# Kernel optimization log

Hardware: AMD Instinct MI355X
Metric: run time of the kernel (lower is better)

The kernel has to match this reference:

```python
import jax, jax.numpy as jnp
import numpy as np

NUM_HEADS = 16

def setup_inputs() -> dict:
    key = jax.random.key(0)
    k1, k2, k3 = jax.random.split(key, 3)
    B, S, D = 4, 2048, 1024
    x = jax.random.normal(k1, (B, S, D), dtype=jnp.float32)
    # xavier-uniform-like small init so unscaled logits stay numerically sane
    w_qkv = jax.random.normal(k2, (3 * D, D), dtype=jnp.float32) * 0.02
    w_out = jax.random.normal(k3, (D, D), dtype=jnp.float32) * 0.02
    return {"x": x, "w_qkv": w_qkv, "w_out": w_out}

def reference(x, w_qkv, w_out):
    B, S, D = x.shape
    H = NUM_HEADS
    d = D // H
    # qkv projection (Linear, no bias): x @ W^T -> [B, S, 3D]
    qkv = jnp.einsum('bsd,ed->bse', x, w_qkv).reshape(B, S, H, 3 * d)
    q, k, v = jnp.split(qkv, 3, axis=-1)           # each [B, S, H, d]
    q = q.transpose(0, 2, 1, 3)                    # [B, H, S, d]
    k = k.transpose(0, 2, 1, 3)
    v = v.transpose(0, 2, 1, 3)
    # NOTE: the original module does NOT scale by 1/sqrt(d) — faithful.
    logits = jnp.einsum('bhqd,bhkd->bhqk', q, k)   # [B, H, S, S]
    attn = jax.nn.softmax(logits, axis=-1)
    vals = jnp.einsum('bhqk,bhkd->bhqd', attn, v)  # [B, H, S, d]
    vals = vals.transpose(0, 2, 1, 3).reshape(B, S, D)
    return jnp.einsum('bsd,od->bso', vals, w_out)
```

## Files before the change

kernel.cpp:

```cpp
#include <hip/hip_runtime.h>
#include <hip/hip_bf16.h>

#define DEVINL __device__ __forceinline__

typedef short bf16x4 __attribute__((ext_vector_type(4)));
typedef short bf16x8 __attribute__((ext_vector_type(8)));
typedef float f32x4 __attribute__((ext_vector_type(4)));
typedef float f32x16 __attribute__((ext_vector_type(16)));
typedef unsigned short us4 __attribute__((ext_vector_type(4)));


DEVINL unsigned short f2bf(float f) {
  unsigned u = __builtin_bit_cast(unsigned, f);
  unsigned r = u + 0x7fffu + ((u >> 16) & 1u);
  return (unsigned short)(r >> 16);
}

DEVINL f32x4 mfma32(bf16x8 a, bf16x8 b, f32x4 c) {
  return __builtin_amdgcn_mfma_f32_16x16x32_bf16(a, b, c, 0, 0, 0);
}

DEVINL f32x16 mfma3216(bf16x8 a, bf16x8 b, f32x16 c) {
  return __builtin_amdgcn_mfma_f32_32x32x16_bf16(a, b, c, 0, 0, 0);
}

DEVINL float fexp2(float x) {
#if __has_builtin(__builtin_amdgcn_exp2f)
  return __builtin_amdgcn_exp2f(x);
#else
  return exp2f(x);
#endif
}

DEVINL unsigned cvt_pk_bf16(float a, float b) {
  unsigned r;
  asm("v_cvt_pk_bf16_f32 %0, %1, %2" : "=v"(r) : "v"(a), "v"(b));
  return r;
}

DEVINL void permswap(unsigned& x, unsigned& y) {
#if __has_builtin(__builtin_amdgcn_permlane32_swap)
  typedef int i32x2_t __attribute__((ext_vector_type(2)));
  i32x2_t r = __builtin_amdgcn_permlane32_swap((int)x, (int)y, false, false);
  x = (unsigned)r[0];
  y = (unsigned)r[1];
#else
  asm("v_permlane32_swap_b32 %0, %1" : "+v"(x), "+v"(y));
#endif
}

#define GLOAD_LDS16(g, l)                                                    \
  __builtin_amdgcn_global_load_lds(                                          \
      (__attribute__((address_space(1))) void*)(unsigned short*)(g),         \
      (__attribute__((address_space(3))) void*)(l), 16, 0, 0)

__global__ void cvtk(const float* __restrict__ src,
                     unsigned short* __restrict__ dst, int n4) {
  int i = blockIdx.x * 256 + threadIdx.x;
  const int st = gridDim.x * 256;
  for (; i < n4; i += st) {
    const float4 v = ((const float4*)src)[i];
    us4 o;
    o[0] = f2bf(v.x); o[1] = f2bf(v.y); o[2] = f2bf(v.z); o[3] = f2bf(v.w);
    ((us4*)dst)[i] = o;
  }
}

__global__ __launch_bounds__(256, 2) void qkv_gemm(
    const unsigned short* __restrict__ A,
    const unsigned short* __restrict__ Bw,
    unsigned short* __restrict__ Qo,
    unsigned short* __restrict__ Ko,
    unsigned short* __restrict__ VTo) {
  constexpr int K = 1024;
  __shared__ unsigned short SH[16384];
  const int tid = threadIdx.x;
  const int lane = tid & 63;
  const int wid = tid >> 6;
  const int l15 = lane & 15, g = lane >> 4;
  const int fid = blockIdx.y * 24 + blockIdx.x;
  const int swzid = (fid & 7) * 192 + (fid >> 3);
  const int m0 = (swzid / 24) * 128;
  const int n0 = (swzid % 24) * 128;
  const int wr = wid >> 1, wc = wid & 1;

  f32x4 acc[4][4] = {};

  const int sidx0 = tid * 8;
  const int sidx1 = (256 + tid) * 8;
  const int r0 = sidx0 >> 5, c0 = sidx0 & 31;
  const int r1 = sidx1 >> 5, c1 = sidx1 & 31;

#define QSTAGE(kt, bb)                                                       \
  {                                                                          \
    const int k0_ = (kt)*32;                                                 \
    GLOAD_LDS16(A + (size_t)(m0 + r0) * K + k0_ + c0,                        \
                SH + (bb)*8192 + sidx0);                                     \
    GLOAD_LDS16(Bw + (size_t)(n0 + r0) * K + k0_ + c0,                       \
                SH + (bb)*8192 + 4096 + sidx0);                              \
    GLOAD_LDS16(A + (size_t)(m0 + r1) * K + k0_ + c1,                        \
                SH + (bb)*8192 + sidx1);                                     \
    GLOAD_LDS16(Bw + (size_t)(n0 + r1) * K + k0_ + c1,                       \
                SH + (bb)*8192 + 4096 + sidx1);                              \
  }

  QSTAGE(0, 0);
  __syncthreads();

  for (int t = 0; t < 32; ++t) {
    const int cb = t & 1;
    if (t < 31) QSTAGE(t + 1, cb ^ 1);
    bf16x8 af[4], bfr[4];
#pragma unroll
    for (int i = 0; i < 4; ++i) {
      af[i] =
          *(const bf16x8*)(SH + cb * 8192 + (wr * 64 + i * 16 + l15) * 32 +
                           g * 8);
      bfr[i] = *(const bf16x8*)(SH + cb * 8192 + 4096 +
                                (wc * 64 + i * 16 + l15) * 32 + g * 8);
    }
#pragma unroll
    for (int mi = 0; mi < 4; ++mi)
#pragma unroll
      for (int ni = 0; ni < 4; ++ni)
        acc[mi][ni] = mfma32(af[mi], bfr[ni], acc[mi][ni]);
    __syncthreads();
  }
#undef QSTAGE

#pragma unroll
  for (int ni = 0; ni < 4; ++ni) {
    const int ebase = n0 + wc * 64 + ni * 16;
    const int h = ebase / 192;
    const int rbase = ebase - h * 192;
#pragma unroll
    for (int mi = 0; mi < 4; ++mi) {
      const int mbase = m0 + wr * 64 + mi * 16 + g * 4;
      if (rbase >= 128) {
        const int rv = rbase + l15 - 128;
        const int b = mbase >> 11, s = mbase & 2047;
        const int bh = b * 16 + h;
        us4 ov;
#pragma unroll
        for (int j = 0; j < 4; ++j) ov[j] = f2bf(acc[mi][ni][j]);
        *(us4*)(VTo + ((size_t)bh * 64 + rv) * 2048 + s) = ov;
      } else {
        const float scale = (rbase < 64) ? 1.44269504f : 1.0f;
        const int eloc = wc * 64 + ni * 16 + l15;
        const int mloc = wr * 64 + mi * 16 + g * 4;
#pragma unroll
        for (int j = 0; j < 4; ++j)
          SH[(mloc + j) * 128 + eloc] = f2bf(acc[mi][ni][j] * scale);
      }
    }
  }
  __syncthreads();
#pragma unroll
  for (int k = 0; k < 8; ++k) {
    const int c = tid + k * 256;
    const int ml = c >> 4, e8 = (c & 15) * 8;
    const int e0 = n0 + e8;
    const int h = e0 / 192;
    const int r = e0 - h * 192;
    if (r < 128) {
      const int mm = m0 + ml;
      const int b = mm >> 11, s = mm & 2047;
      const int bh = b * 16 + h;
      const bf16x8 v = *(const bf16x8*)&SH[ml * 128 + e8];
      if (r < 64)
        *(bf16x8*)(Qo + ((size_t)bh * 2048 + s) * 64 + r) = v;
      else
        *(bf16x8*)(Ko + ((size_t)bh * 2048 + s) * 64 + (r - 64)) = v;
    }
  }
}

__global__ __launch_bounds__(256, 2) void attn_fwd(
    const unsigned short* __restrict__ Q,
    const unsigned short* __restrict__ K,
    const unsigned short* __restrict__ VT,
    unsigned short* __restrict__ Vals) {
  __shared__ unsigned short Ks[2][128 * 64];
  __shared__ unsigned short Vs[2][64 * 128];
  __shared__ float invs[4][2][32];
  const int tid = threadIdx.x;
  const int lane = tid & 63;
  const int wid = tid >> 6;
  const int l31 = lane & 31;
  const int hi = lane >> 5;
  const int bid = (blockIdx.x & 7) * 64 + (blockIdx.x >> 3);
  const int bh = bid >> 3;
  const int q0 = (bid & 7) * 256 + wid * 64;
  const unsigned short* Qb = Q + (size_t)bh * (2048 * 64);
  const unsigned short* Kb = K + (size_t)bh * (2048 * 64);
  const unsigned short* Vb = VT + (size_t)bh * (64 * 2048);

  bf16x8 qf[2][4];
#pragma unroll
  for (int qt = 0; qt < 2; ++qt) {
    const unsigned short* qrow = Qb + (size_t)(q0 + qt * 32 + l31) * 64;
#pragma unroll
    for (int kw = 0; kw < 4; ++kw)
      qf[qt][kw] = *(const bf16x8*)(qrow + kw * 16 + hi * 8);
  }

  float lsum[2] = {0.0f, 0.0f};
  f32x16 o[2][2] = {};
  const unsigned swz = (unsigned)((l31 & 7) << 4);
  const unsigned laneK = (unsigned)(l31 * 128) + (((unsigned)hi << 4) ^ swz);
  const unsigned laneV = (unsigned)(l31 * 256) + (((unsigned)hi << 4) ^ swz);

#define STAGE(kv0, nb)                                                       \
  {                                                                          \
    _Pragma("unroll") for (int j = 0; j < 4; ++j) {                          \
      const int c = tid + j * 256;                                           \
      const int kr = c >> 3;                                                 \
      const int ksc = ((((c & 7) << 4) ^ ((kr & 7) << 4)) >> 1);             \
      GLOAD_LDS16(Kb + (size_t)((kv0) + kr) * 64 + ksc, &Ks[nb][c * 8]);     \
      const int vr = c >> 4;                                                 \
      const int vsc = ((((c & 15) << 4) ^ ((vr & 7) << 4)) >> 1);            \
      GLOAD_LDS16(Vb + (size_t)vr * 2048 + (kv0) + vsc, &Vs[nb][c * 8]);     \
    }                                                                        \
  }

  STAGE(0, 0);
  __syncthreads();

  for (int kv0 = 0; kv0 < 2048; kv0 += 128) {
    const int cur = (kv0 >> 7) & 1;
    if (kv0 + 128 < 2048) STAGE(kv0 + 128, cur ^ 1);
    const char* kb = (const char*)Ks[cur];
    const char* vb = (const char*)Vs[cur];
#pragma unroll
    for (int sub = 0; sub < 4; ++sub) {
      const unsigned kbase = laneK + (unsigned)(sub * 4096);
      bf16x8 kf[4];
#pragma unroll
      for (int kw = 0; kw < 4; ++kw)
        kf[kw] = *(const bf16x8*)(kb + (kbase ^ (unsigned)(kw * 32)));
      f32x16 s0 = {}, s1 = {};
      __builtin_amdgcn_s_setprio(1);
#pragma unroll
      for (int kw = 0; kw < 4; ++kw) s0 = mfma3216(kf[kw], qf[0][kw], s0);
#pragma unroll
      for (int kw = 0; kw < 4; ++kw) s1 = mfma3216(kf[kw], qf[1][kw], s1);
      __builtin_amdgcn_s_setprio(0);
#pragma unroll
      for (int half = 0; half < 2; ++half) {
        const int pb = half * 8;
        const unsigned ksoff = (unsigned)((sub * 2 + half) * 32);
        const bf16x8 vf0 = *(const bf16x8*)(vb + (laneV ^ ksoff));
        const bf16x8 vf1 = *(const bf16x8*)(vb + ((laneV + 8192u) ^ ksoff));
#pragma unroll
        for (int qt = 0; qt < 2; ++qt) {
          const f32x16& s = qt ? s1 : s0;
          const float p0 = fexp2(s[pb + 0]);
          const float p1 = fexp2(s[pb + 1]);
          const float p2 = fexp2(s[pb + 2]);
          const float p3 = fexp2(s[pb + 3]);
          const float p4 = fexp2(s[pb + 4]);
          const float p5 = fexp2(s[pb + 5]);
          const float p6 = fexp2(s[pb + 6]);
          const float p7 = fexp2(s[pb + 7]);
          lsum[qt] += ((p0 + p1) + (p2 + p3)) + ((p4 + p5) + (p6 + p7));
          unsigned w0 = cvt_pk_bf16(p0, p1);
          unsigned w2 = cvt_pk_bf16(p4, p5);
          permswap(w0, w2);
          unsigned w1 = cvt_pk_bf16(p2, p3);
          unsigned w3 = cvt_pk_bf16(p6, p7);
          permswap(w1, w3);
          union {
            unsigned u[4];
            bf16x8 v;
          } pk;
          pk.u[0] = w0;
          pk.u[1] = w1;
          pk.u[2] = w2;
          pk.u[3] = w3;
          __builtin_amdgcn_s_setprio(1);
          o[qt][0] = mfma3216(pk.v, vf0, o[qt][0]);
          o[qt][1] = mfma3216(pk.v, vf1, o[qt][1]);
          __builtin_amdgcn_s_setprio(0);
        }
      }
    }
    __syncthreads();
  }
#undef STAGE

#pragma unroll
  for (int qt = 0; qt < 2; ++qt) {
    const float ltot = lsum[qt] + __shfl_xor(lsum[qt], 32);
    invs[wid][qt][l31] = 1.0f / ltot;
  }
  const int b = bh >> 4, h = bh & 15;
#pragma unroll
  for (int qt = 0; qt < 2; ++qt) {
    unsigned short* ob =
        Vals + (size_t)(b * 2048 + q0 + qt * 32) * 1024 + h * 64 + l31;
#pragma unroll
    for (int j = 0; j < 16; ++j) {
      const int ql = (j & 3) + 8 * (j >> 2) + 4 * hi;
      const float inv = invs[wid][qt][ql];
      ob[(size_t)ql * 1024] = f2bf(o[qt][0][j] * inv);
      ob[(size_t)ql * 1024 + 32] = f2bf(o[qt][1][j] * inv);
    }
  }
}

__global__ __launch_bounds__(256, 2) void out_gemm(
    const unsigned short* __restrict__ A,
    const unsigned short* __restrict__ Bw,
    float* __restrict__ C) {
  constexpr int K = 1024, BK = 32;
  __shared__ unsigned short As[128 * BK];
  __shared__ unsigned short Bs[128 * BK];
  const int tid = threadIdx.x;
  const int lane = tid & 63;
  const int wid = tid >> 6;
  const int l15 = lane & 15, g = lane >> 4;
  const int fid = blockIdx.y * 8 + blockIdx.x;
  const int swzid = (fid & 7) * 64 + (fid >> 3);
  const int m0 = (swzid >> 3) * 128;
  const int n0 = (swzid & 7) * 128;
  const int wr = wid >> 1, wc = wid & 1;

  f32x4 acc[4][4] = {};

  const int sidx0 = tid * 8;
  const int sidx1 = (256 + tid) * 8;
  const int r0 = sidx0 >> 5, c0 = sidx0 & 31;
  const int r1 = sidx1 >> 5, c1 = sidx1 & 31;

  for (int k0 = 0; k0 < K; k0 += BK) {
    __syncthreads();
    GLOAD_LDS16(A + (size_t)(m0 + r0) * K + k0 + c0, As + sidx0);
    GLOAD_LDS16(Bw + (size_t)(n0 + r0) * K + k0 + c0, Bs + sidx0);
    GLOAD_LDS16(A + (size_t)(m0 + r1) * K + k0 + c1, As + sidx1);
    GLOAD_LDS16(Bw + (size_t)(n0 + r1) * K + k0 + c1, Bs + sidx1);
    __syncthreads();
    bf16x8 af[4], bfr[4];
#pragma unroll
    for (int i = 0; i < 4; ++i) {
      af[i] = *(const bf16x8*)(As + (wr * 64 + i * 16 + l15) * BK + g * 8);
      bfr[i] = *(const bf16x8*)(Bs + (wc * 64 + i * 16 + l15) * BK + g * 8);
    }
#pragma unroll
    for (int mi = 0; mi < 4; ++mi)
#pragma unroll
      for (int ni = 0; ni < 4; ++ni)
        acc[mi][ni] = mfma32(af[mi], bfr[ni], acc[mi][ni]);
  }

#pragma unroll
  for (int mi = 0; mi < 4; ++mi) {
    const int mbase = m0 + wr * 64 + mi * 16 + g * 4;
#pragma unroll
    for (int ni = 0; ni < 4; ++ni) {
      const int n = n0 + wc * 64 + ni * 16 + l15;
#pragma unroll
      for (int j = 0; j < 4; ++j)
        C[(size_t)(mbase + j) * 1024 + n] = acc[mi][ni][j];
    }
  }
}

extern "C" void kernel_launch(void* const* d_in, const int* in_sizes, int n_in,
                              void* d_out, int out_size, void* d_ws,
                              size_t ws_size, hipStream_t stream) {
  const float* x = (const float*)d_in[0];
  const float* w_qkv = (const float*)d_in[1];
  const float* w_out = (const float*)d_in[2];
  float* out = (float*)d_out;

  char* ws = (char*)d_ws;
  unsigned short* xb = (unsigned short*)(ws);
  unsigned short* wqkvb = (unsigned short*)(ws + (16u << 20));
  unsigned short* woutb = (unsigned short*)(ws + (22u << 20));
  unsigned short* Qt = (unsigned short*)(ws + (24u << 20));
  unsigned short* Kt = (unsigned short*)(ws + (40u << 20));
  unsigned short* VTt = (unsigned short*)(ws + (56u << 20));
  unsigned short* vals = xb;

  cvtk<<<2048, 256, 0, stream>>>(x, xb, 8388608 / 4);
  cvtk<<<2048, 256, 0, stream>>>(w_qkv, wqkvb, 3145728 / 4);
  cvtk<<<1024, 256, 0, stream>>>(w_out, woutb, 1048576 / 4);
  qkv_gemm<<<dim3(24, 64), 256, 0, stream>>>(xb, wqkvb, Qt, Kt, VTt);
  attn_fwd<<<512, 256, 0, stream>>>(Qt, Kt, VTt, vals);
  out_gemm<<<dim3(8, 64), 256, 0, stream>>>(vals, woutb, out);
}
```

Baseline: 186.5 us.

## Use eight waves per attention block with one 32-row query tile each

The attention kernel moves from 4 waves each handling two 32-row query tiles to 8 waves each handling one 32-row tile. The block still covers 256 query rows and shares the same K/V LDS staging, now split across 512 threads. Per-wave register use drops, so more waves can be resident to hide latency. The cost is more waves contending for LDS reads and barriers, and the K fragments loaded from LDS are reused over half as many query rows.

```diff
diff --git a/kernel.cpp b/kernel.cpp
--- a/kernel.cpp
+++ b/kernel.cpp
@@ -175,14 +175,14 @@
   }
 }
 
-__global__ __launch_bounds__(256, 2) void attn_fwd(
+__global__ __launch_bounds__(512, 4) void attn_fwd(
     const unsigned short* __restrict__ Q,
     const unsigned short* __restrict__ K,
     const unsigned short* __restrict__ VT,
     unsigned short* __restrict__ Vals) {
   __shared__ unsigned short Ks[2][128 * 64];
   __shared__ unsigned short Vs[2][64 * 128];
-  __shared__ float invs[4][2][32];
+  __shared__ float invs[8][32];
   const int tid = threadIdx.x;
   const int lane = tid & 63;
   const int wid = tid >> 6;
@@ -190,30 +190,27 @@
   const int hi = lane >> 5;
   const int bid = (blockIdx.x & 7) * 64 + (blockIdx.x >> 3);
   const int bh = bid >> 3;
-  const int q0 = (bid & 7) * 256 + wid * 64;
+  const int q0 = (bid & 7) * 256 + wid * 32;
   const unsigned short* Qb = Q + (size_t)bh * (2048 * 64);
   const unsigned short* Kb = K + (size_t)bh * (2048 * 64);
   const unsigned short* Vb = VT + (size_t)bh * (64 * 2048);
 
-  bf16x8 qf[2][4];
-#pragma unroll
-  for (int qt = 0; qt < 2; ++qt) {
-    const unsigned short* qrow = Qb + (size_t)(q0 + qt * 32 + l31) * 64;
-#pragma unroll
-    for (int kw = 0; kw < 4; ++kw)
-      qf[qt][kw] = *(const bf16x8*)(qrow + kw * 16 + hi * 8);
-  }
-
-  float lsum[2] = {0.0f, 0.0f};
-  f32x16 o[2][2] = {};
+  const unsigned short* qrow = Qb + (size_t)(q0 + l31) * 64;
+  bf16x8 qf[4];
+#pragma unroll
+  for (int kw = 0; kw < 4; ++kw)
+    qf[kw] = *(const bf16x8*)(qrow + kw * 16 + hi * 8);
+
+  float lsum = 0.0f;
+  f32x16 o0 = {}, o1 = {};
   const unsigned swz = (unsigned)((l31 & 7) << 4);
   const unsigned laneK = (unsigned)(l31 * 128) + (((unsigned)hi << 4) ^ swz);
   const unsigned laneV = (unsigned)(l31 * 256) + (((unsigned)hi << 4) ^ swz);
 
 #define STAGE(kv0, nb)                                                       \
   {                                                                          \
-    _Pragma("unroll") for (int j = 0; j < 4; ++j) {                          \
-      const int c = tid + j * 256;                                           \
+    _Pragma("unroll") for (int j = 0; j < 2; ++j) {                          \
+      const int c = tid + j * 512;                                           \
       const int kr = c >> 3;                                                 \
       const int ksc = ((((c & 7) << 4) ^ ((kr & 7) << 4)) >> 1);             \
       GLOAD_LDS16(Kb + (size_t)((kv0) + kr) * 64 + ksc, &Ks[nb][c * 8]);     \
@@ -238,12 +235,10 @@
 #pragma unroll
       for (int kw = 0; kw < 4; ++kw)
         kf[kw] = *(const bf16x8*)(kb + (kbase ^ (unsigned)(kw * 32)));
-      f32x16 s0 = {}, s1 = {};
+      f32x16 s = {};
       __builtin_amdgcn_s_setprio(1);
 #pragma unroll
-      for (int kw = 0; kw < 4; ++kw) s0 = mfma3216(kf[kw], qf[0][kw], s0);
-#pragma unroll
-      for (int kw = 0; kw < 4; ++kw) s1 = mfma3216(kf[kw], qf[1][kw], s1);
+      for (int kw = 0; kw < 4; ++kw) s = mfma3216(kf[kw], qf[kw], s);
       __builtin_amdgcn_s_setprio(0);
 #pragma unroll
       for (int half = 0; half < 2; ++half) {
@@ -251,60 +246,49 @@
         const unsigned ksoff = (unsigned)((sub * 2 + half) * 32);
         const bf16x8 vf0 = *(const bf16x8*)(vb + (laneV ^ ksoff));
         const bf16x8 vf1 = *(const bf16x8*)(vb + ((laneV + 8192u) ^ ksoff));
-#pragma unroll
-        for (int qt = 0; qt < 2; ++qt) {
-          const f32x16& s = qt ? s1 : s0;
-          const float p0 = fexp2(s[pb + 0]);
-          const float p1 = fexp2(s[pb + 1]);
-          const float p2 = fexp2(s[pb + 2]);
-          const float p3 = fexp2(s[pb + 3]);
-          const float p4 = fexp2(s[pb + 4]);
-          const float p5 = fexp2(s[pb + 5]);
-          const float p6 = fexp2(s[pb + 6]);
-          const float p7 = fexp2(s[pb + 7]);
-          lsum[qt] += ((p0 + p1) + (p2 + p3)) + ((p4 + p5) + (p6 + p7));
-          unsigned w0 = cvt_pk_bf16(p0, p1);
-          unsigned w2 = cvt_pk_bf16(p4, p5);
-          permswap(w0, w2);
-          unsigned w1 = cvt_pk_bf16(p2, p3);
-          unsigned w3 = cvt_pk_bf16(p6, p7);
-          permswap(w1, w3);
-          union {
-            unsigned u[4];
-            bf16x8 v;
-          } pk;
-          pk.u[0] = w0;
-          pk.u[1] = w1;
-          pk.u[2] = w2;
-          pk.u[3] = w3;
-          __builtin_amdgcn_s_setprio(1);
-          o[qt][0] = mfma3216(pk.v, vf0, o[qt][0]);
-          o[qt][1] = mfma3216(pk.v, vf1, o[qt][1]);
-          __builtin_amdgcn_s_setprio(0);
-        }
+        const float p0 = fexp2(s[pb + 0]);
+        const float p1 = fexp2(s[pb + 1]);
+        const float p2 = fexp2(s[pb + 2]);
+        const float p3 = fexp2(s[pb + 3]);
+        const float p4 = fexp2(s[pb + 4]);
+        const float p5 = fexp2(s[pb + 5]);
+        const float p6 = fexp2(s[pb + 6]);
+        const float p7 = fexp2(s[pb + 7]);
+        lsum += ((p0 + p1) + (p2 + p3)) + ((p4 + p5) + (p6 + p7));
+        unsigned w0 = cvt_pk_bf16(p0, p1);
+        unsigned w2 = cvt_pk_bf16(p4, p5);
+        permswap(w0, w2);
+        unsigned w1 = cvt_pk_bf16(p2, p3);
+        unsigned w3 = cvt_pk_bf16(p6, p7);
+        permswap(w1, w3);
+        union {
+          unsigned u[4];
+          bf16x8 v;
+        } pk;
+        pk.u[0] = w0;
+        pk.u[1] = w1;
+        pk.u[2] = w2;
+        pk.u[3] = w3;
+        __builtin_amdgcn_s_setprio(1);
+        o0 = mfma3216(pk.v, vf0, o0);
+        o1 = mfma3216(pk.v, vf1, o1);
+        __builtin_amdgcn_s_setprio(0);
       }
     }
     __syncthreads();
   }
 #undef STAGE
 
-#pragma unroll
-  for (int qt = 0; qt < 2; ++qt) {
-    const float ltot = lsum[qt] + __shfl_xor(lsum[qt], 32);
-    invs[wid][qt][l31] = 1.0f / ltot;
-  }
+  const float ltot = lsum + __shfl_xor(lsum, 32);
+  invs[wid][l31] = 1.0f / ltot;
   const int b = bh >> 4, h = bh & 15;
-#pragma unroll
-  for (int qt = 0; qt < 2; ++qt) {
-    unsigned short* ob =
-        Vals + (size_t)(b * 2048 + q0 + qt * 32) * 1024 + h * 64 + l31;
-#pragma unroll
-    for (int j = 0; j < 16; ++j) {
-      const int ql = (j & 3) + 8 * (j >> 2) + 4 * hi;
-      const float inv = invs[wid][qt][ql];
-      ob[(size_t)ql * 1024] = f2bf(o[qt][0][j] * inv);
-      ob[(size_t)ql * 1024 + 32] = f2bf(o[qt][1][j] * inv);
-    }
+  unsigned short* ob = Vals + (size_t)(b * 2048 + q0) * 1024 + h * 64 + l31;
+#pragma unroll
+  for (int j = 0; j < 16; ++j) {
+    const int ql = (j & 3) + 8 * (j >> 2) + 4 * hi;
+    const float inv = invs[wid][ql];
+    ob[(size_t)ql * 1024] = f2bf(o0[j] * inv);
+    ob[(size_t)ql * 1024 + 32] = f2bf(o1[j] * inv);
   }
 }
 
@@ -386,6 +370,6 @@
   cvtk<<<2048, 256, 0, stream>>>(w_qkv, wqkvb, 3145728 / 4);
   cvtk<<<1024, 256, 0, stream>>>(w_out, woutb, 1048576 / 4);
   qkv_gemm<<<dim3(24, 64), 256, 0, stream>>>(xb, wqkvb, Qt, Kt, VTt);
-  attn_fwd<<<512, 256, 0, stream>>>(Qt, Kt, VTt, vals);
+  attn_fwd<<<512, 512, 0, stream>>>(Qt, Kt, VTt, vals);
   out_gemm<<<dim3(8, 64), 256, 0, stream>>>(vals, woutb, out);
 }
```

Measured after the change: 187.2 us. About the same (+0.4%).
